# Optimization experiments

Measured on AMD Instinct MI355X. Metric: run time of the kernel, lower is better.

Reference implementation:

```python
import jax, jax.numpy as jnp
import numpy as np
from jax import lax

# QKeras quantized_bits(8, 0, alpha=1, keep_negative=1):
#   delta = 2^-(bits-1) = 1/128, q(x) = clip(round(x*128), -128, 127)/128
QB_SCALE = 128.0
# QKeras quantized_relu(8, 0): q(x) = clip(round(x*256), 0, 255)/256
QR_SCALE = 256.0

def _ste(q, x):
    # straight-through estimator: forward = q(x), backward = identity
    return x + lax.stop_gradient(q - x)

def qbits(x):
    q = jnp.clip(jnp.round(x * QB_SCALE), -QB_SCALE, QB_SCALE - 1.0) / QB_SCALE
    return _ste(q, x)

def qrelu(x):
    q = jnp.clip(jnp.round(x * QR_SCALE), 0.0, QR_SCALE - 1.0) / QR_SCALE
    return _ste(q, x)


def setup_inputs() -> dict:
    key = jax.random.key(0)
    ks = jax.random.split(key, 9)
    B, C, F = 1000000, 16, 3
    dims = [C * F, 64, 32, 32]
    x = jax.random.normal(ks[0], (B, C, F), dtype=jnp.float32)
    def w(k, i, o):
        return jax.random.normal(k, (i, o), dtype=jnp.float32) * (0.5 / np.sqrt(i))
    inp = {"x": x}
    for li in range(3):
        inp[f"w{li+1}"] = w(ks[1 + 2 * li], dims[li], dims[li + 1])
        inp[f"b{li+1}"] = jax.random.normal(ks[2 + 2 * li], (dims[li + 1],), dtype=jnp.float32) * 0.05
    inp["wout"] = w(ks[7], dims[-1], 5)
    inp["bout"] = jax.random.normal(ks[8], (5,), dtype=jnp.float32) * 0.05
    return inp


def reference(x, w1, b1, w2, b2, w3, b3, wout, bout):
    h = x.reshape(x.shape[0], -1)  # Flatten: [B, 48]
    for w, b in ((w1, b1), (w2, b2), (w3, b3)):
        # QDense: fake-quantize kernel & bias, fp32 matmul, quantized_relu
        h = qrelu(h @ qbits(w) + qbits(b))
    return h @ wout + bout  # final float Dense -> logits [B, 5]
```

## Files before the change

kernel.cpp:

```cpp
#include <hip/hip_runtime.h>
#include <hip/hip_bf16.h>

typedef short  short8 __attribute__((ext_vector_type(8)));
typedef float  f32x4  __attribute__((ext_vector_type(4)));
typedef unsigned int u32;
typedef unsigned long long u64;
typedef unsigned short u16;

__device__ __forceinline__ u32 f2bf(float v) {
    u32 u = __float_as_uint(v);
    return (u + 0x7FFFu + ((u >> 16) & 1u)) >> 16;
}
__device__ __forceinline__ float qround128(float w) {
    float q = rintf(w * 128.0f);
    return fminf(fmaxf(q, -128.0f), 127.0f);
}
__device__ __forceinline__ u32 cvtpk(float a, float b) {
    __hip_bfloat162 h = __float22bfloat162_rn(make_float2(a, b));
    union { __hip_bfloat162 h; u32 u; } cv; cv.h = h; return cv.u;
}
__device__ __forceinline__ u64 qrelu_pack4(f32x4 a) {
    float q0 = fminf(fmaxf(rintf(a[0]), 0.f), 255.f);
    float q1 = fminf(fmaxf(rintf(a[1]), 0.f), 255.f);
    float q2 = fminf(fmaxf(rintf(a[2]), 0.f), 255.f);
    float q3 = fminf(fmaxf(rintf(a[3]), 0.f), 255.f);
    return (u64)cvtpk(q0, q1) | ((u64)cvtpk(q2, q3) << 32);
}
union FragU { short8 s; u32 u[4]; };
__device__ __forceinline__ f32x4 mfma16(short8 a, short8 b, f32x4 c) {
    return __builtin_amdgcn_mfma_f32_16x16x32_bf16(a, b, c, 0, 0, 0);
}


__global__ void prep(const float* __restrict__ w1, const float* __restrict__ b1,
                     const float* __restrict__ w2, const float* __restrict__ b2,
                     const float* __restrict__ w3, const float* __restrict__ b3,
                     const float* __restrict__ wo, const float* __restrict__ bo,
                     u16* __restrict__ wsh) {
    int t = threadIdx.x;
    for (int idx = t; idx < 16 * 512; idx += 256) {
        int blk = idx >> 9, e = idx & 511;
        int l = e >> 3, j = e & 7;
        int r  = l & 15;
        int kk = ((l >> 4) << 3) + j;
        float val = 0.f;
        if (blk < 8) {
            int mt = blk >> 1, ks = blk & 1;
            int k = ks * 32 + kk, fo = mt * 16 + r;
            if (k < 48) val = 2.0f * qround128(w1[k * 64 + fo]);
        } else if (blk < 12) {
            int bi = blk - 8, mt = bi >> 1, ks = bi & 1;
            int k = ks * 32 + kk, fo = mt * 16 + r;
            val = qround128(w2[k * 32 + fo]) * (1.0f / 128.0f);
        } else if (blk < 14) {
            int mt = blk - 12;
            val = qround128(w3[kk * 32 + mt * 16 + r]) * (1.0f / 128.0f);
        } else {
            float wv = (r < 5) ? wo[kk * 5 + r] * (1.0f / 256.0f) : 0.f;
            u32 hb = f2bf(wv);
            if (blk == 14) { wsh[idx] = (u16)hb; continue; }
            val = wv - __uint_as_float(hb << 16);
        }
        wsh[idx] = (u16)f2bf(val);
    }
    float* wsf = (float*)(wsh + 8192);
    for (int i = t; i < 64; i += 256) wsf[i]       = 2.0f * qround128(b1[i]);
    for (int i = t; i < 32; i += 256) wsf[64 + i]  = 2.0f * qround128(b2[i]);
    for (int i = t; i < 32; i += 256) wsf[96 + i]  = 2.0f * qround128(b3[i]);
    for (int i = t; i < 16; i += 256) wsf[128 + i] = (i < 5) ? bo[i] : 0.f;
}


__global__ __launch_bounds__(256, 2) void mlp_mfma(const float* __restrict__ x,
                                                   const u16* __restrict__ wsh,
                                                   float* __restrict__ out, int ntiles) {
    __shared__ __align__(16) u16 smem[4][3840];
    const int tid = threadIdx.x;
    const int wid = tid >> 6, lane = tid & 63;
    const int c = lane & 15, g = lane >> 4;

    short8 wf[16];
    const short8* wv = (const short8*)wsh;
    #pragma unroll
    for (int i = 0; i < 16; ++i) wf[i] = wv[i * 64 + lane];

    const float* wsf = (const float*)(wsh + 8192);
    f32x4 b1q[4], b2q[2], b3q[2], boq;
    #pragma unroll
    for (int i = 0; i < 4; ++i) b1q[i] = *(const f32x4*)(wsf + i * 16 + 4 * g);
    #pragma unroll
    for (int i = 0; i < 2; ++i) b2q[i] = *(const f32x4*)(wsf + 64 + i * 16 + 4 * g);
    #pragma unroll
    for (int i = 0; i < 2; ++i) b3q[i] = *(const f32x4*)(wsf + 96 + i * 16 + 4 * g);
    boq = *(const f32x4*)(wsf + 128 + 4 * g);

    u16* H = &smem[wid][0];
    const int xoff = c * 48 + g * 8;

    const int gw = blockIdx.x * 4 + wid;
    const int nw = gridDim.x * 4;

    const float* xl = x + (size_t)gw * 768 + xoff;
    float4 xa = *(const float4*)(xl);
    float4 xb = *(const float4*)(xl + 4);
    float4 xc = {0.f, 0.f, 0.f, 0.f}, xd = {0.f, 0.f, 0.f, 0.f};
    if (g < 2) { xc = *(const float4*)(xl + 32); xd = *(const float4*)(xl + 36); }

    for (int t0 = gw; t0 < ntiles; t0 += nw) {
        const int t1 = t0 + nw;
        const bool have = t1 < ntiles;
        float4 na, nb, nc, nd;
        if (have) {
            const float* nl = x + (size_t)t1 * 768 + xoff;
            na = *(const float4*)(nl);
            nb = *(const float4*)(nl + 4);
            if (g < 2) { nc = *(const float4*)(nl + 32); nd = *(const float4*)(nl + 36); }
        }

        float v0[8] = {xa.x, xa.y, xa.z, xa.w, xb.x, xb.y, xb.z, xb.w};
        float v1[8] = {xc.x, xc.y, xc.z, xc.w, xd.x, xd.y, xd.z, xd.w};
        FragU bh0, bl0, bh1, bl1;
        #pragma unroll
        for (int p = 0; p < 4; ++p) {
            u32 u = cvtpk(v0[2 * p], v0[2 * p + 1]);
            bh0.u[p] = u;
            float r0 = v0[2 * p]     - __uint_as_float(u << 16);
            float r1 = v0[2 * p + 1] - __uint_as_float(u & 0xFFFF0000u);
            bl0.u[p] = cvtpk(r0, r1);
            u32 w = cvtpk(v1[2 * p], v1[2 * p + 1]);
            bh1.u[p] = w;
            float s0 = v1[2 * p]     - __uint_as_float(w << 16);
            float s1 = v1[2 * p + 1] - __uint_as_float(w & 0xFFFF0000u);
            bl1.u[p] = cvtpk(s0, s1);
        }

        #pragma unroll
        for (int mt = 0; mt < 4; ++mt) {
            f32x4 a = b1q[mt];
            a = mfma16(wf[mt * 2 + 0], bh0.s, a);
            a = mfma16(wf[mt * 2 + 1], bh1.s, a);
            a = mfma16(wf[mt * 2 + 0], bl0.s, a);
            a = mfma16(wf[mt * 2 + 1], bl1.s, a);
            *(u64*)(H + c * 80 + mt * 16 + 4 * g) = qrelu_pack4(a);
        }

        short8 p0 = *(const short8*)(H + c * 80 + 8 * g);
        short8 p1 = *(const short8*)(H + c * 80 + 32 + 8 * g);
        #pragma unroll
        for (int mt = 0; mt < 2; ++mt) {
            f32x4 a = b2q[mt];
            a = mfma16(wf[8 + mt * 2 + 0], p0, a);
            a = mfma16(wf[8 + mt * 2 + 1], p1, a);
            *(u64*)(H + 1280 + c * 80 + mt * 16 + 4 * g) = qrelu_pack4(a);
        }

        short8 p2 = *(const short8*)(H + 1280 + c * 80 + 8 * g);
        #pragma unroll
        for (int mt = 0; mt < 2; ++mt) {
            f32x4 a = b3q[mt];
            a = mfma16(wf[12 + mt], p2, a);
            *(u64*)(H + 2560 + c * 80 + mt * 16 + 4 * g) = qrelu_pack4(a);
        }

        short8 p3 = *(const short8*)(H + 2560 + c * 80 + 8 * g);
        f32x4 ao = boq;
        ao = mfma16(wf[14], p3, ao);
        ao = mfma16(wf[15], p3, ao);

        float* orow = out + (size_t)t0 * 80 + c * 5;
        if (g == 0) {
            orow[0] = ao[0]; orow[1] = ao[1]; orow[2] = ao[2]; orow[3] = ao[3];
        } else if (g == 1) {
            orow[4] = ao[0];
        }

        if (have) { xa = na; xb = nb; if (g < 2) { xc = nc; xd = nd; } }
    }
}

extern "C" void kernel_launch(void* const* d_in, const int* in_sizes, int n_in,
                              void* d_out, int out_size, void* d_ws, size_t ws_size,
                              hipStream_t stream) {
    const float* x  = (const float*)d_in[0];
    const float* w1 = (const float*)d_in[1];
    const float* b1 = (const float*)d_in[2];
    const float* w2 = (const float*)d_in[3];
    const float* b2 = (const float*)d_in[4];
    const float* w3 = (const float*)d_in[5];
    const float* b3 = (const float*)d_in[6];
    const float* wo = (const float*)d_in[7];
    const float* bo = (const float*)d_in[8];
    float* out = (float*)d_out;

    int B = in_sizes[0] / 48;
    int ntiles = B / 16;

    prep<<<1, 256, 0, stream>>>(w1, b1, w2, b2, w3, b3, wo, bo, (u16*)d_ws);

    int blocks = (ntiles + 3) / 4;
    if (blocks > 2048) blocks = 2048;
    mlp_mfma<<<blocks, 256, 0, stream>>>(x, (const u16*)d_ws, out, ntiles);
}
```

Measured before the change: 60.39 us.

## Process two tiles per wave iteration with interleaved layers and padded LDS rows

Each wave now handles a pair of 16-row tiles per loop iteration. It loads both inputs up front and runs each MLP layer for both tiles back-to-back, giving independent MFMA chains and LDS traffic that can overlap. The register-prefetch of the next tile is removed in favour of this intra-iteration ILP. LDS row stride changes from 80 to 88 halves to reduce bank conflicts, and the per-wave LDS footprint doubles. Launch sizing is switched to count pairs.

```diff
diff --git a/kernel.cpp b/kernel.cpp
--- a/kernel.cpp
+++ b/kernel.cpp
@@ -30,7 +30,6 @@
 __device__ __forceinline__ f32x4 mfma16(short8 a, short8 b, f32x4 c) {
     return __builtin_amdgcn_mfma_f32_16x16x32_bf16(a, b, c, 0, 0, 0);
 }
-
 
 __global__ void prep(const float* __restrict__ w1, const float* __restrict__ b1,
                      const float* __restrict__ w2, const float* __restrict__ b2,
@@ -71,10 +70,13 @@
 }
 
 
+#define RS 88
+#define SLAB 4224
+
 __global__ __launch_bounds__(256, 2) void mlp_mfma(const float* __restrict__ x,
                                                    const u16* __restrict__ wsh,
                                                    float* __restrict__ out, int ntiles) {
-    __shared__ __align__(16) u16 smem[4][3840];
+    __shared__ __align__(16) u16 smem[4][2][SLAB];
     const int tid = threadIdx.x;
     const int wid = tid >> 6, lane = tid & 63;
     const int c = lane & 15, g = lane >> 4;
@@ -94,87 +96,101 @@
     for (int i = 0; i < 2; ++i) b3q[i] = *(const f32x4*)(wsf + 96 + i * 16 + 4 * g);
     boq = *(const f32x4*)(wsf + 128 + 4 * g);
 
-    u16* H = &smem[wid][0];
     const int xoff = c * 48 + g * 8;
-
+    const int npairs = (ntiles + 1) >> 1;
     const int gw = blockIdx.x * 4 + wid;
     const int nw = gridDim.x * 4;
 
-    const float* xl = x + (size_t)gw * 768 + xoff;
-    float4 xa = *(const float4*)(xl);
-    float4 xb = *(const float4*)(xl + 4);
-    float4 xc = {0.f, 0.f, 0.f, 0.f}, xd = {0.f, 0.f, 0.f, 0.f};
-    if (g < 2) { xc = *(const float4*)(xl + 32); xd = *(const float4*)(xl + 36); }
-
-    for (int t0 = gw; t0 < ntiles; t0 += nw) {
-        const int t1 = t0 + nw;
-        const bool have = t1 < ntiles;
-        float4 na, nb, nc, nd;
-        if (have) {
-            const float* nl = x + (size_t)t1 * 768 + xoff;
-            na = *(const float4*)(nl);
-            nb = *(const float4*)(nl + 4);
-            if (g < 2) { nc = *(const float4*)(nl + 32); nd = *(const float4*)(nl + 36); }
-        }
-
-        float v0[8] = {xa.x, xa.y, xa.z, xa.w, xb.x, xb.y, xb.z, xb.w};
-        float v1[8] = {xc.x, xc.y, xc.z, xc.w, xd.x, xd.y, xd.z, xd.w};
-        FragU bh0, bl0, bh1, bl1;
-        #pragma unroll
-        for (int p = 0; p < 4; ++p) {
-            u32 u = cvtpk(v0[2 * p], v0[2 * p + 1]);
-            bh0.u[p] = u;
-            float r0 = v0[2 * p]     - __uint_as_float(u << 16);
-            float r1 = v0[2 * p + 1] - __uint_as_float(u & 0xFFFF0000u);
-            bl0.u[p] = cvtpk(r0, r1);
-            u32 w = cvtpk(v1[2 * p], v1[2 * p + 1]);
-            bh1.u[p] = w;
-            float s0 = v1[2 * p]     - __uint_as_float(w << 16);
-            float s1 = v1[2 * p + 1] - __uint_as_float(w & 0xFFFF0000u);
-            bl1.u[p] = cvtpk(s0, s1);
-        }
-
-        #pragma unroll
-        for (int mt = 0; mt < 4; ++mt) {
-            f32x4 a = b1q[mt];
-            a = mfma16(wf[mt * 2 + 0], bh0.s, a);
-            a = mfma16(wf[mt * 2 + 1], bh1.s, a);
-            a = mfma16(wf[mt * 2 + 0], bl0.s, a);
-            a = mfma16(wf[mt * 2 + 1], bl1.s, a);
-            *(u64*)(H + c * 80 + mt * 16 + 4 * g) = qrelu_pack4(a);
-        }
-
-        short8 p0 = *(const short8*)(H + c * 80 + 8 * g);
-        short8 p1 = *(const short8*)(H + c * 80 + 32 + 8 * g);
-        #pragma unroll
-        for (int mt = 0; mt < 2; ++mt) {
-            f32x4 a = b2q[mt];
-            a = mfma16(wf[8 + mt * 2 + 0], p0, a);
-            a = mfma16(wf[8 + mt * 2 + 1], p1, a);
-            *(u64*)(H + 1280 + c * 80 + mt * 16 + 4 * g) = qrelu_pack4(a);
-        }
-
-        short8 p2 = *(const short8*)(H + 1280 + c * 80 + 8 * g);
-        #pragma unroll
-        for (int mt = 0; mt < 2; ++mt) {
-            f32x4 a = b3q[mt];
-            a = mfma16(wf[12 + mt], p2, a);
-            *(u64*)(H + 2560 + c * 80 + mt * 16 + 4 * g) = qrelu_pack4(a);
-        }
-
-        short8 p3 = *(const short8*)(H + 2560 + c * 80 + 8 * g);
-        f32x4 ao = boq;
-        ao = mfma16(wf[14], p3, ao);
-        ao = mfma16(wf[15], p3, ao);
-
-        float* orow = out + (size_t)t0 * 80 + c * 5;
-        if (g == 0) {
-            orow[0] = ao[0]; orow[1] = ao[1]; orow[2] = ao[2]; orow[3] = ao[3];
-        } else if (g == 1) {
-            orow[4] = ao[0];
-        }
-
-        if (have) { xa = na; xb = nb; if (g < 2) { xc = nc; xd = nd; } }
+    for (int p = gw; p < npairs; p += nw) {
+        int tt[2];
+        tt[0] = 2 * p;
+        tt[1] = (2 * p + 1 < ntiles) ? (2 * p + 1) : (2 * p);
+
+        float4 xa[2], xb[2], xc[2], xd[2];
+        #pragma unroll
+        for (int u = 0; u < 2; ++u) {
+            const float* xl = x + (size_t)tt[u] * 768 + xoff;
+            xa[u] = *(const float4*)(xl);
+            xb[u] = *(const float4*)(xl + 4);
+            xc[u] = make_float4(0.f, 0.f, 0.f, 0.f);
+            xd[u] = make_float4(0.f, 0.f, 0.f, 0.f);
+            if (g < 2) { xc[u] = *(const float4*)(xl + 32); xd[u] = *(const float4*)(xl + 36); }
+        }
+
+        FragU bh0[2], bl0[2], bh1[2], bl1[2];
+        #pragma unroll
+        for (int u = 0; u < 2; ++u) {
+            float v0[8] = {xa[u].x, xa[u].y, xa[u].z, xa[u].w, xb[u].x, xb[u].y, xb[u].z, xb[u].w};
+            float v1[8] = {xc[u].x, xc[u].y, xc[u].z, xc[u].w, xd[u].x, xd[u].y, xd[u].z, xd[u].w};
+            #pragma unroll
+            for (int q = 0; q < 4; ++q) {
+                u32 uu = cvtpk(v0[2 * q], v0[2 * q + 1]);
+                bh0[u].u[q] = uu;
+                float r0 = v0[2 * q]     - __uint_as_float(uu << 16);
+                float r1 = v0[2 * q + 1] - __uint_as_float(uu & 0xFFFF0000u);
+                bl0[u].u[q] = cvtpk(r0, r1);
+                u32 ww = cvtpk(v1[2 * q], v1[2 * q + 1]);
+                bh1[u].u[q] = ww;
+                float s0 = v1[2 * q]     - __uint_as_float(ww << 16);
+                float s1 = v1[2 * q + 1] - __uint_as_float(ww & 0xFFFF0000u);
+                bl1[u].u[q] = cvtpk(s0, s1);
+            }
+        }
+
+        #pragma unroll
+        for (int u = 0; u < 2; ++u) {
+            u16* H = &smem[wid][u][0];
+            #pragma unroll
+            for (int mt = 0; mt < 4; ++mt) {
+                f32x4 a = b1q[mt];
+                a = mfma16(wf[mt * 2 + 0], bh0[u].s, a);
+                a = mfma16(wf[mt * 2 + 1], bh1[u].s, a);
+                a = mfma16(wf[mt * 2 + 0], bl0[u].s, a);
+                a = mfma16(wf[mt * 2 + 1], bl1[u].s, a);
+                *(u64*)(H + c * RS + mt * 16 + 4 * g) = qrelu_pack4(a);
+            }
+        }
+
+        #pragma unroll
+        for (int u = 0; u < 2; ++u) {
+            u16* H = &smem[wid][u][0];
+            short8 p0 = *(const short8*)(H + c * RS + 8 * g);
+            short8 p1 = *(const short8*)(H + c * RS + 32 + 8 * g);
+            #pragma unroll
+            for (int mt = 0; mt < 2; ++mt) {
+                f32x4 a = b2q[mt];
+                a = mfma16(wf[8 + mt * 2 + 0], p0, a);
+                a = mfma16(wf[8 + mt * 2 + 1], p1, a);
+                *(u64*)(H + 16 * RS + c * RS + mt * 16 + 4 * g) = qrelu_pack4(a);
+            }
+        }
+
+        #pragma unroll
+        for (int u = 0; u < 2; ++u) {
+            u16* H = &smem[wid][u][0];
+            short8 p2 = *(const short8*)(H + 16 * RS + c * RS + 8 * g);
+            #pragma unroll
+            for (int mt = 0; mt < 2; ++mt) {
+                f32x4 a = b3q[mt];
+                a = mfma16(wf[12 + mt], p2, a);
+                *(u64*)(H + 32 * RS + c * RS + mt * 16 + 4 * g) = qrelu_pack4(a);
+            }
+        }
+
+        #pragma unroll
+        for (int u = 0; u < 2; ++u) {
+            u16* H = &smem[wid][u][0];
+            short8 p3 = *(const short8*)(H + 32 * RS + c * RS + 8 * g);
+            f32x4 ao = boq;
+            ao = mfma16(wf[14], p3, ao);
+            ao = mfma16(wf[15], p3, ao);
+            float* orow = out + (size_t)tt[u] * 80 + c * 5;
+            if (g == 0) {
+                orow[0] = ao[0]; orow[1] = ao[1]; orow[2] = ao[2]; orow[3] = ao[3];
+            } else if (g == 1) {
+                orow[4] = ao[0];
+            }
+        }
     }
 }
 
@@ -197,7 +213,8 @@
 
     prep<<<1, 256, 0, stream>>>(w1, b1, w2, b2, w3, b3, wo, bo, (u16*)d_ws);
 
-    int blocks = (ntiles + 3) / 4;
+    int npairs = (ntiles + 1) / 2;
+    int blocks = (npairs + 3) / 4;
     if (blocks > 2048) blocks = 2048;
     mlp_mfma<<<blocks, 256, 0, stream>>>(x, (const u16*)d_ws, out, ntiles);
 }
```

Measured after the change: 68.88 us. +14.1%, slower.

## Drop register prefetch, raise occupancy, split MFMA accumulation chains

Applied to the files above, without the earlier changes.

Removes the software prefetch of the next tile's x into registers and instead loads the current tile at the top of each loop iteration. Launch bounds go from 2 to 3 blocks per SIMD so that more waves can hide memory latency. The dependent MFMA accumulation chains are split into independent accumulators that are summed afterwards, which shortens the dependency chains. This trades explicit prefetching for latency hiding through occupancy, and the changed summation order may slightly alter rounding before quantization.

```diff
diff --git a/kernel.cpp b/kernel.cpp
--- a/kernel.cpp
+++ b/kernel.cpp
@@ -30,7 +30,6 @@
 __device__ __forceinline__ f32x4 mfma16(short8 a, short8 b, f32x4 c) {
     return __builtin_amdgcn_mfma_f32_16x16x32_bf16(a, b, c, 0, 0, 0);
 }
-
 
 __global__ void prep(const float* __restrict__ w1, const float* __restrict__ b1,
                      const float* __restrict__ w2, const float* __restrict__ b2,
@@ -71,7 +70,7 @@
 }
 
 
-__global__ __launch_bounds__(256, 2) void mlp_mfma(const float* __restrict__ x,
+__global__ __launch_bounds__(256, 3) void mlp_mfma(const float* __restrict__ x,
                                                    const u16* __restrict__ wsh,
                                                    float* __restrict__ out, int ntiles) {
     __shared__ __align__(16) u16 smem[4][3840];
@@ -100,47 +99,40 @@
     const int gw = blockIdx.x * 4 + wid;
     const int nw = gridDim.x * 4;
 
-    const float* xl = x + (size_t)gw * 768 + xoff;
-    float4 xa = *(const float4*)(xl);
-    float4 xb = *(const float4*)(xl + 4);
-    float4 xc = {0.f, 0.f, 0.f, 0.f}, xd = {0.f, 0.f, 0.f, 0.f};
-    if (g < 2) { xc = *(const float4*)(xl + 32); xd = *(const float4*)(xl + 36); }
-
     for (int t0 = gw; t0 < ntiles; t0 += nw) {
-        const int t1 = t0 + nw;
-        const bool have = t1 < ntiles;
-        float4 na, nb, nc, nd;
-        if (have) {
-            const float* nl = x + (size_t)t1 * 768 + xoff;
-            na = *(const float4*)(nl);
-            nb = *(const float4*)(nl + 4);
-            if (g < 2) { nc = *(const float4*)(nl + 32); nd = *(const float4*)(nl + 36); }
-        }
+        const float* xl = x + (size_t)t0 * 768 + xoff;
+        float4 xa = *(const float4*)(xl);
+        float4 xb = *(const float4*)(xl + 4);
+        float4 xc = make_float4(0.f, 0.f, 0.f, 0.f);
+        float4 xd = make_float4(0.f, 0.f, 0.f, 0.f);
+        if (g < 2) { xc = *(const float4*)(xl + 32); xd = *(const float4*)(xl + 36); }
 
         float v0[8] = {xa.x, xa.y, xa.z, xa.w, xb.x, xb.y, xb.z, xb.w};
         float v1[8] = {xc.x, xc.y, xc.z, xc.w, xd.x, xd.y, xd.z, xd.w};
         FragU bh0, bl0, bh1, bl1;
         #pragma unroll
         for (int p = 0; p < 4; ++p) {
-            u32 u = cvtpk(v0[2 * p], v0[2 * p + 1]);
-            bh0.u[p] = u;
-            float r0 = v0[2 * p]     - __uint_as_float(u << 16);
-            float r1 = v0[2 * p + 1] - __uint_as_float(u & 0xFFFF0000u);
+            u32 uu = cvtpk(v0[2 * p], v0[2 * p + 1]);
+            bh0.u[p] = uu;
+            float r0 = v0[2 * p]     - __uint_as_float(uu << 16);
+            float r1 = v0[2 * p + 1] - __uint_as_float(uu & 0xFFFF0000u);
             bl0.u[p] = cvtpk(r0, r1);
-            u32 w = cvtpk(v1[2 * p], v1[2 * p + 1]);
-            bh1.u[p] = w;
-            float s0 = v1[2 * p]     - __uint_as_float(w << 16);
-            float s1 = v1[2 * p + 1] - __uint_as_float(w & 0xFFFF0000u);
+            u32 ww = cvtpk(v1[2 * p], v1[2 * p + 1]);
+            bh1.u[p] = ww;
+            float s0 = v1[2 * p]     - __uint_as_float(ww << 16);
+            float s1 = v1[2 * p + 1] - __uint_as_float(ww & 0xFFFF0000u);
             bl1.u[p] = cvtpk(s0, s1);
         }
 
         #pragma unroll
         for (int mt = 0; mt < 4; ++mt) {
-            f32x4 a = b1q[mt];
-            a = mfma16(wf[mt * 2 + 0], bh0.s, a);
-            a = mfma16(wf[mt * 2 + 1], bh1.s, a);
-            a = mfma16(wf[mt * 2 + 0], bl0.s, a);
-            a = mfma16(wf[mt * 2 + 1], bl1.s, a);
+            f32x4 ah = b1q[mt];
+            ah = mfma16(wf[mt * 2 + 0], bh0.s, ah);
+            ah = mfma16(wf[mt * 2 + 1], bh1.s, ah);
+            f32x4 al = {0.f, 0.f, 0.f, 0.f};
+            al = mfma16(wf[mt * 2 + 0], bl0.s, al);
+            al = mfma16(wf[mt * 2 + 1], bl1.s, al);
+            f32x4 a = ah + al;
             *(u64*)(H + c * 80 + mt * 16 + 4 * g) = qrelu_pack4(a);
         }
 
@@ -148,9 +140,11 @@
         short8 p1 = *(const short8*)(H + c * 80 + 32 + 8 * g);
         #pragma unroll
         for (int mt = 0; mt < 2; ++mt) {
-            f32x4 a = b2q[mt];
-            a = mfma16(wf[8 + mt * 2 + 0], p0, a);
-            a = mfma16(wf[8 + mt * 2 + 1], p1, a);
+            f32x4 a0 = b2q[mt];
+            a0 = mfma16(wf[8 + mt * 2 + 0], p0, a0);
+            f32x4 a1 = {0.f, 0.f, 0.f, 0.f};
+            a1 = mfma16(wf[8 + mt * 2 + 1], p1, a1);
+            f32x4 a = a0 + a1;
             *(u64*)(H + 1280 + c * 80 + mt * 16 + 4 * g) = qrelu_pack4(a);
         }
 
@@ -163,9 +157,11 @@
         }
 
         short8 p3 = *(const short8*)(H + 2560 + c * 80 + 8 * g);
-        f32x4 ao = boq;
-        ao = mfma16(wf[14], p3, ao);
-        ao = mfma16(wf[15], p3, ao);
+        f32x4 aoh = boq;
+        aoh = mfma16(wf[14], p3, aoh);
+        f32x4 aol = {0.f, 0.f, 0.f, 0.f};
+        aol = mfma16(wf[15], p3, aol);
+        f32x4 ao = aoh + aol;
 
         float* orow = out + (size_t)t0 * 80 + c * 5;
         if (g == 0) {
@@ -173,8 +169,6 @@
         } else if (g == 1) {
             orow[4] = ao[0];
         }
-
-        if (have) { xa = na; xb = nb; if (g < 2) { xc = nc; xd = nd; } }
     }
 }
 
```

After: 62.70 us. 1.04x slower.
